# Kernel tuning notes

Hardware: AMD Instinct MI355X
Metric: run time of the kernel (lower is better)

## Reference

```python
import jax, jax.numpy as jnp
import numpy as np
from jax.ops import segment_sum

N_NODES = 10000
N_EDGES = 160000
HIDDEN = 128
NUM_RBF = 32
NUM_LAYERS = 2
LATENT = 64
N_GRAPHS = 128
CUTOFF = 5.0
EPS = 1e-8


def expnorm_rbf(r):
    # ExpNormalSmearing (ViSNet default RBF) with cosine cutoff
    means = jnp.linspace(jnp.exp(-CUTOFF), 1.0, NUM_RBF)          # [R]
    beta = (2.0 / NUM_RBF * (1.0 - jnp.exp(-CUTOFF))) ** -2
    cut = 0.5 * (jnp.cos(jnp.pi * r / CUTOFF) + 1.0) * (r < CUTOFF)
    return cut[:, None] * jnp.exp(-beta * (jnp.exp(-r)[:, None] - means) ** 2)  # [E,R]


def setup_inputs() -> dict:
    key = jax.random.key(0)
    ks = jax.random.split(key, 16)
    z = jax.random.randint(ks[0], (N_NODES,), 0, 100)
    pos = jax.random.normal(ks[1], (N_NODES, 3), jnp.float32) * 2.0
    batch = jnp.sort(jax.random.randint(ks[2], (N_NODES,), 0, N_GRAPHS))
    edge_index = jax.random.randint(ks[3], (2, N_EDGES), 0, N_NODES)
    H, R, L = HIDDEN, NUM_RBF, NUM_LAYERS
    s = lambda fan: 1.0 / np.sqrt(fan)
    embed_table = jax.random.normal(ks[4], (100, H), jnp.float32)
    W_rbf = jax.random.normal(ks[5], (L, R, H), jnp.float32) * s(R)
    W1 = jax.random.normal(ks[6], (L, H, H), jnp.float32) * s(H)
    Wo = jax.random.normal(ks[7], (L, H, H), jnp.float32) * s(H)
    Wv = jax.random.normal(ks[8], (L, H, H), jnp.float32) * s(H)
    Wvec1 = jax.random.normal(ks[9], (H, H), jnp.float32) * s(H)
    Wvec2 = jax.random.normal(ks[10], (H, H), jnp.float32) * s(H)
    W_a = jax.random.normal(ks[11], (2 * H, H), jnp.float32) * s(2 * H)
    b_a = jnp.zeros((H,), jnp.float32)
    W_b = jax.random.normal(ks[12], (H, LATENT + 1), jnp.float32) * s(H)
    b_b = jnp.zeros((LATENT + 1,), jnp.float32)
    # MSE-stability init fix from the torch module:
    # scalar_linear.bias[-1] = -1.0 ; scalar_linear.weight[-1] *= 0.1
    b_b = b_b.at[-1].set(-1.0)
    W_b = W_b.at[:, -1].multiply(0.1)
    return dict(z=z, pos=pos, batch=batch, edge_index=edge_index,
                embed_table=embed_table, W_rbf=W_rbf, W1=W1, Wo=Wo, Wv=Wv,
                Wvec1=Wvec1, Wvec2=Wvec2, W_a=W_a, b_a=b_a, W_b=W_b, b_b=b_b)


def reference(z, pos, batch, edge_index, embed_table, W_rbf, W1, Wo, Wv,
              Wvec1, Wvec2, W_a, b_a, W_b, b_b):
    src, dst = edge_index[0], edge_index[1]
    # edge geometry (computed once, shared across layers)
    d = pos[dst] - pos[src]                      # [E,3]
    r = jnp.sqrt(jnp.sum(d * d, axis=-1) + EPS)  # [E]
    dirn = d / r[:, None]                        # [E,3]
    rbf = expnorm_rbf(r)                         # [E,R]

    x = embed_table[z]                           # [N,H] scalar features
    vec = jnp.zeros((x.shape[0], 3, HIDDEN), x.dtype)  # [N,3,H] equivariant features

    for l in range(NUM_LAYERS):
        filt = rbf @ W_rbf[l]                                        # [E,H] radial filter
        phi = jax.nn.silu((x[src] * filt) @ W1[l])                   # [E,H] edge message
        dx = segment_sum(phi, dst, num_segments=N_NODES)             # scatter-add
        x = x + dx @ Wo[l]
        vmix = jnp.einsum('nch,hk->nck', vec, Wv[l])                 # [N,3,H]
        vmsg = vmix[src] * filt[:, None, :] + phi[:, None, :] * dirn[:, :, None]  # [E,3,H]
        vec = vec + segment_sum(vmsg, dst, num_segments=N_NODES)

    # gated-equivariant output head (pre_reduce -> [N, latent+1] scalars)
    v2 = jnp.einsum('nch,hk->nck', vec, Wvec2)
    vnorm = jnp.sqrt(jnp.sum(v2 * v2, axis=1) + EPS)                 # [N,H]
    a = jax.nn.silu(jnp.concatenate([x, vnorm], axis=-1) @ W_a + b_a)
    out = a @ W_b + b_b                                              # [N, latent+1]

    pooled = segment_sum(out, batch, num_segments=N_GRAPHS)          # global_add_pool
    mu = pooled[:, :LATENT]
    log_var = jnp.clip(pooled[:, LATENT:LATENT + 1], -10.0, 2.0)
    return mu, log_var
```

## Files before the change

kernel.cpp:

```cpp
#include <hip/hip_runtime.h>
#include <math.h>

#define N_NODES 10000
#define N_EDGES 160000
#define HIDDEN 128
#define NUM_RBF 32
#define LATENT 64
#define N_GRAPHS 128
#define CUTOFF 5.0f
#define EPS 1e-8f

#define NBLK_N 157

typedef __attribute__((ext_vector_type(8))) short short8;
typedef __attribute__((ext_vector_type(4))) float f32x4;
typedef unsigned short ushort_t;

__device__ __forceinline__ float fast_silu(float v) {
    return v * __builtin_amdgcn_rcpf(1.0f + __expf(-v));
}

__device__ __forceinline__ ushort_t f2bf(float f) {
    union { float f; unsigned u; } v;
    v.f = f;
    unsigned r = v.u + 0x7FFFu + ((v.u >> 16) & 1u);
    return (ushort_t)(r >> 16);
}
__device__ __forceinline__ float bf2f(ushort_t u) {
    union { unsigned u; float f; } v;
    v.u = ((unsigned)u) << 16;
    return v.f;
}

__global__ void init_kernel(const int* __restrict__ z, const float* __restrict__ embed,
                            float* __restrict__ x, ushort_t* __restrict__ x16,
                            float* __restrict__ vec, float* __restrict__ dxb,
                            float* __restrict__ pooled, int* __restrict__ deg,
                            const float* __restrict__ W1, const float* __restrict__ Wrbf,
                            const float* __restrict__ Wv, const float* __restrict__ Wo,
                            const float* __restrict__ Wvec2, const float* __restrict__ W_a,
                            const float* __restrict__ W_b, ushort_t* __restrict__ W1T,
                            ushort_t* __restrict__ WrbfT, ushort_t* __restrict__ WvT,
                            ushort_t* __restrict__ WoT, ushort_t* __restrict__ Wvec2T,
                            ushort_t* __restrict__ W_aT, ushort_t* __restrict__ W_bT) {
    if (blockIdx.x < 15000) {
        int i = blockIdx.x * 256 + threadIdx.x;
        if (i < N_NODES * 384) vec[i] = 0.0f;
        if (i < N_NODES * 128) {
            float v = embed[z[i >> 7] * 128 + (i & 127)];
            x[i] = v;
            x16[i] = f2bf(v);
            dxb[i] = 0.0f;
        }
        if (i < N_NODES) deg[i] = 0;
        if (i < N_GRAPHS * (LATENT + 1)) pooled[i] = 0.0f;
        return;
    }
    int i = (blockIdx.x - 15000) * 256 + threadIdx.x;
    if (i < 2 * 128 * 128) {
        int l = i >> 14;
        int n = (i & 16383) >> 7;
        int k = i & 127;
        W1T[i] = f2bf(W1[l * 16384 + k * 128 + n]);
        WvT[i] = f2bf(Wv[l * 16384 + k * 128 + n]);
        WoT[i] = f2bf(Wo[l * 16384 + k * 128 + n]);
    }
    if (i < 2 * 128 * 32) {
        int l = i >> 12;
        int n = (i & 4095) >> 5;
        int k = i & 31;
        WrbfT[i] = f2bf(Wrbf[l * 4096 + k * 128 + n]);
    }
    if (i < 128 * 128) {
        int n = i >> 7;
        int k = i & 127;
        Wvec2T[i] = f2bf(Wvec2[k * 128 + n]);
    }
    if (i < 128 * 256) {
        int n = i >> 8;
        int k = i & 255;
        W_aT[i] = f2bf(W_a[k * 128 + n]);
    }
    if (i < 80 * 128) {
        int n = i >> 7;
        int k = i & 127;
        W_bT[i] = (n < LATENT + 1) ? f2bf(W_b[k * (LATENT + 1) + n]) : (ushort_t)0;
    }
}

__global__ void hist_kernel(const int* __restrict__ dst, int* __restrict__ deg) {
    int e = blockIdx.x * blockDim.x + threadIdx.x;
    if (e < N_EDGES) atomicAdd(&deg[dst[e]], 1);
}

__global__ void prefix_kernel(const int* __restrict__ deg, int* __restrict__ cursor) {
    __shared__ int part[1024];
    const int ITEMS = 10;
    int t = threadIdx.x;
    int base = t * ITEMS;
    int local[ITEMS];
    int s = 0;
#pragma unroll
    for (int j = 0; j < ITEMS; j++) {
        int idx = base + j;
        int v = (idx < N_NODES) ? deg[idx] : 0;
        local[j] = s;
        s += v;
    }
    part[t] = s;
    __syncthreads();
    for (int off = 1; off < 1024; off <<= 1) {
        int v = (t >= off) ? part[t - off] : 0;
        __syncthreads();
        part[t] += v;
        __syncthreads();
    }
    int base_sum = (t > 0) ? part[t - 1] : 0;
#pragma unroll
    for (int j = 0; j < ITEMS; j++) {
        int idx = base + j;
        if (idx < N_NODES) cursor[idx] = base_sum + local[j];
    }
}

__global__ void scatter_geom_kernel(const int* __restrict__ ei, const float* __restrict__ pos,
                                    int* __restrict__ cursor, int* __restrict__ sperm,
                                    int* __restrict__ dperm, ushort_t* __restrict__ rbf16,
                                    float* __restrict__ dirn) {
    int e = blockIdx.x * blockDim.x + threadIdx.x;
    if (e >= N_EDGES) return;
    int s = ei[e];
    int t = ei[N_EDGES + e];
    int p = atomicAdd(&cursor[t], 1);
    sperm[p] = s;
    dperm[p] = t;

    float dx = pos[t * 3 + 0] - pos[s * 3 + 0];
    float dy = pos[t * 3 + 1] - pos[s * 3 + 1];
    float dz = pos[t * 3 + 2] - pos[s * 3 + 2];
    float r = sqrtf(dx * dx + dy * dy + dz * dz + EPS);
    float inv = 1.0f / r;
    dirn[p * 3 + 0] = dx * inv;
    dirn[p * 3 + 1] = dy * inv;
    dirn[p * 3 + 2] = dz * inv;

    float e5 = __expf(-CUTOFF);
    float span = 1.0f - e5;
    float b = (2.0f / NUM_RBF) * span;
    float beta = 1.0f / (b * b);
    float cut = (r < CUTOFF) ? 0.5f * (__cosf((float)M_PI * r / CUTOFF) + 1.0f) : 0.0f;
    float er = __expf(-r);
#pragma unroll
    for (int k = 0; k < NUM_RBF; k++) {
        float mean = e5 + span * ((float)k / (NUM_RBF - 1));
        float d = er - mean;
        rbf16[(size_t)p * 32 + k] = f2bf(cut * __expf(-beta * d * d));
    }
}

template <int K, int EPI>
__device__ __forceinline__ void gemm_body(ushort_t* As, float* __restrict__ A,
                                          const ushort_t* __restrict__ WT,
                                          const float* __restrict__ bias,
                                          const float* __restrict__ Cin, float* __restrict__ C,
                                          ushort_t* __restrict__ C16, int M, int bx, int tid) {
    constexpr int STR = K + 8;
    int row0 = bx * 64;
    int w = tid >> 6;
    int lane = tid & 63;
    int c = lane & 15;
    int q = lane >> 4;
    int wr0 = w * 16;

    {
        int r = wr0 + (lane >> 2);
        int row = row0 + r;
        int segbase = (lane & 3) * (K / 4);
#pragma unroll
        for (int u = 0; u < K / 16; u++) {
            int k0 = segbase + u * 4;
            float4 v = make_float4(0.f, 0.f, 0.f, 0.f);
            if (row < M) v = *(const float4*)(A + (size_t)row * 128 + k0);
            ushort_t b4[4] = {f2bf(v.x), f2bf(v.y), f2bf(v.z), f2bf(v.w)};
            *(uint2*)(As + r * STR + k0) = *(uint2*)b4;
        }
        if ((EPI & 16) && row < M) {
            float4 z4 = make_float4(0.f, 0.f, 0.f, 0.f);
#pragma unroll
            for (int u = 0; u < 8; u++)
                *(float4*)(A + (size_t)row * 128 + (lane & 3) * 32 + u * 4) = z4;
        }
    }

    f32x4 acc[8] = {};
#pragma unroll
    for (int s = 0; s < K / 32; s++) {
        short8 af = *(const short8*)(As + (wr0 + c) * STR + s * 32 + q * 8);
#pragma unroll
        for (int t8 = 0; t8 < 8; t8++) {
            short8 bf = *(const short8*)(WT + (size_t)(t8 * 16 + c) * K + s * 32 + q * 8);
            acc[t8] = __builtin_amdgcn_mfma_f32_16x16x32_bf16(af, bf, acc[t8], 0, 0, 0);
        }
    }

    if (EPI & 8) {
#pragma unroll
        for (int t8 = 0; t8 < 8; t8++) {
#pragma unroll
            for (int r4 = 0; r4 < 4; r4++) {
                int lrow = wr0 + q * 4 + r4;
                As[lrow * STR + t8 * 16 + c] = f2bf(acc[t8][r4]);
            }
        }
#pragma unroll
        for (int i = 0; i < 4; i++) {
            int slot = lane + i * 64;
            int rl = slot >> 4;
            int c8 = slot & 15;
            int row = row0 + wr0 + rl;
            if (row < M)
                *(uint4*)((ushort_t*)C + (size_t)row * 128 + c8 * 8) =
                    *(uint4*)(As + (wr0 + rl) * STR + c8 * 8);
        }
    } else {
#pragma unroll
        for (int t8 = 0; t8 < 8; t8++) {
#pragma unroll
            for (int r4 = 0; r4 < 4; r4++) {
                int row = row0 + wr0 + q * 4 + r4;
                if (row < M) {
                    int col = t8 * 16 + c;
                    float o = acc[t8][r4];
                    if (EPI & 1) o += bias[col];
                    if (EPI & 2) o += Cin[(size_t)row * 128 + col];
                    if (EPI & 4) o = fast_silu(o);
                    C[(size_t)row * 128 + col] = o;
                    if (EPI & 64) C16[(size_t)row * 128 + col] = f2bf(o);
                }
            }
        }
    }
}

__global__ __launch_bounds__(256, 4) void combo1_kernel(float* __restrict__ dxb,
                                                        const ushort_t* __restrict__ WoT0,
                                                        float* __restrict__ x,
                                                        ushort_t* __restrict__ x16,
                                                        float* __restrict__ vec,
                                                        const ushort_t* __restrict__ WvT1,
                                                        ushort_t* __restrict__ vmix16) {
    __shared__ ushort_t As[64 * 136];
    if (blockIdx.x < NBLK_N)
        gemm_body<128, 2 | 16 | 64>(As, dxb, WoT0, nullptr, x, x, x16, N_NODES, blockIdx.x,
                                    threadIdx.x);
    else
        gemm_body<128, 8>(As, vec, WvT1, nullptr, nullptr, (float*)vmix16, nullptr, N_NODES * 3,
                          blockIdx.x - NBLK_N, threadIdx.x);
}

__global__ __launch_bounds__(256, 4) void combo2_kernel(float* __restrict__ dxb,
                                                        const ushort_t* __restrict__ WoT1,
                                                        float* __restrict__ x,
                                                        float* __restrict__ vec,
                                                        const ushort_t* __restrict__ Wvec2T,
                                                        float* __restrict__ vbuf) {
    __shared__ ushort_t As[64 * 136];
    if (blockIdx.x < NBLK_N)
        gemm_body<128, 2>(As, dxb, WoT1, nullptr, x, x, nullptr, N_NODES, blockIdx.x,
                          threadIdx.x);
    else
        gemm_body<128, 0>(As, vec, Wvec2T, nullptr, nullptr, vbuf, nullptr, N_NODES * 3,
                          blockIdx.x - NBLK_N, threadIdx.x);
}

__global__ __launch_bounds__(256) void wa_pool_kernel(const float* __restrict__ x,
                                                      const float* __restrict__ vbuf,
                                                      const ushort_t* __restrict__ W_aT,
                                                      const float* __restrict__ b_a,
                                                      const ushort_t* __restrict__ W_bT,
                                                      const float* __restrict__ b_b,
                                                      const int* __restrict__ batch,
                                                      float* __restrict__ pooled) {
    __shared__ ushort_t As[16 * 264];
    __shared__ ushort_t A2[16 * 136];
    __shared__ int s_b[16];
    int tid = threadIdx.x;
    int row0 = blockIdx.x * 16;
    int w = tid >> 6;
    int lane = tid & 63;
    int c = lane & 15;
    int q = lane >> 4;

    if (tid < 16) s_b[tid] = batch[row0 + tid];
    {
        int r = tid >> 4;
        int seg = (tid & 15) * 16;
        int row = row0 + r;
#pragma unroll
        for (int u = 0; u < 4; u++) {
            int k0 = seg + u * 4;
            float4 v;
            if (k0 >= 128) {
                const float* vb = vbuf + (size_t)row * 384 + (k0 - 128);
                float4 va = *(const float4*)(vb);
                float4 vb2 = *(const float4*)(vb + 128);
                float4 vc = *(const float4*)(vb + 256);
                v.x = sqrtf(va.x * va.x + vb2.x * vb2.x + vc.x * vc.x + EPS);
                v.y = sqrtf(va.y * va.y + vb2.y * vb2.y + vc.y * vc.y + EPS);
                v.z = sqrtf(va.z * va.z + vb2.z * vb2.z + vc.z * vc.z + EPS);
                v.w = sqrtf(va.w * va.w + vb2.w * vb2.w + vc.w * vc.w + EPS);
            } else {
                v = *(const float4*)(x + (size_t)row * 128 + k0);
            }
            ushort_t b4[4] = {f2bf(v.x), f2bf(v.y), f2bf(v.z), f2bf(v.w)};
            *(uint2*)(As + r * 264 + k0) = *(uint2*)b4;
        }
    }
    __syncthreads();

    f32x4 acc[2] = {};
#pragma unroll
    for (int s = 0; s < 8; s++) {
        short8 af = *(const short8*)(As + c * 264 + s * 32 + q * 8);
#pragma unroll
        for (int i = 0; i < 2; i++) {
            int t8 = 2 * w + i;
            short8 bf = *(const short8*)(W_aT + (size_t)(t8 * 16 + c) * 256 + s * 32 + q * 8);
            acc[i] = __builtin_amdgcn_mfma_f32_16x16x32_bf16(af, bf, acc[i], 0, 0, 0);
        }
    }
#pragma unroll
    for (int i = 0; i < 2; i++) {
#pragma unroll
        for (int r4 = 0; r4 < 4; r4++) {
            int col = (2 * w + i) * 16 + c;
            A2[(q * 4 + r4) * 136 + col] = f2bf(fast_silu(acc[i][r4] + b_a[col]));
        }
    }
    __syncthreads();

    for (int t5 = w; t5 < 5; t5 += 4) {
        f32x4 acc2 = {};
#pragma unroll
        for (int s = 0; s < 4; s++) {
            short8 af = *(const short8*)(A2 + c * 136 + s * 32 + q * 8);
            short8 bf = *(const short8*)(W_bT + (size_t)(t5 * 16 + c) * 128 + s * 32 + q * 8);
            acc2 = __builtin_amdgcn_mfma_f32_16x16x32_bf16(af, bf, acc2, 0, 0, 0);
        }
        int col = t5 * 16 + c;
        if (col < LATENT + 1) {
            float bb = b_b[col];
#pragma unroll
            for (int r4 = 0; r4 < 4; r4++)
                atomicAdd(&pooled[s_b[q * 4 + r4] * (LATENT + 1) + col], acc2[r4] + bb);
        }
    }
}

template <bool HASV>
__global__ __launch_bounds__(256, 4) void edge_fused(
    const ushort_t* __restrict__ rbf16, const ushort_t* __restrict__ WrbfT,
    const ushort_t* __restrict__ x16, const int* __restrict__ sperm,
    const int* __restrict__ dperm, const ushort_t* __restrict__ W1T,
    const float* __restrict__ dirn, const ushort_t* __restrict__ vmix,
    float* __restrict__ dxb, float* __restrict__ vec) {
    __shared__ __align__(16) char smem_raw[HASV ? 36864 : 18432];
    ushort_t* Ts = (ushort_t*)smem_raw;
    ushort_t* PhiT = (ushort_t*)smem_raw;
    ushort_t* FiltT = (ushort_t*)(smem_raw + 18432);
    __shared__ __align__(16) int s_src[64];
    __shared__ __align__(16) int s_dst[64];
    __shared__ __align__(16) float s_dir4[256];

    int tid = threadIdx.x;
    int row0 = blockIdx.x * 64;
    int w = tid >> 6;
    int lane = tid & 63;
    int c = lane & 15;
    int q = lane >> 4;
    int wr0 = w * 16;

    if (lane < 16) {
        s_src[wr0 + lane] = sperm[row0 + wr0 + lane];
        s_dst[wr0 + lane] = dperm[row0 + wr0 + lane];
    }
    if (w == 3) {
        const float* dp = dirn + (size_t)(row0 + lane) * 3;
        s_dir4[lane * 4 + 0] = dp[0];
        s_dir4[lane * 4 + 1] = dp[1];
        s_dir4[lane * 4 + 2] = dp[2];
        s_dir4[lane * 4 + 3] = 0.f;
    }

    int srow[4];
#pragma unroll
    for (int r = 0; r < 4; r++) srow[r] = sperm[row0 + wr0 + q * 4 + r];
    ushort_t xv[4][8];
#pragma unroll
    for (int r = 0; r < 4; r++) {
        const ushort_t* xp = x16 + (size_t)srow[r] * 128 + c;
#pragma unroll
        for (int t8 = 0; t8 < 8; t8++) xv[r][t8] = xp[t8 * 16];
    }

    f32x4 facc[8];
    {
        short8 af = *(const short8*)(rbf16 + (size_t)(row0 + wr0 + c) * 32 + q * 8);
#pragma unroll
        for (int t8 = 0; t8 < 8; t8++) {
            short8 bfr = *(const short8*)(WrbfT + (size_t)(t8 * 16 + c) * 32 + q * 8);
            f32x4 z = {};
            facc[t8] = __builtin_amdgcn_mfma_f32_16x16x32_bf16(af, bfr, z, 0, 0, 0);
        }
    }

#pragma unroll
    for (int t8 = 0; t8 < 8; t8++) {
#pragma unroll
        for (int r = 0; r < 4; r++) {
            int row = wr0 + q * 4 + r;
            Ts[row * 136 + t8 * 16 + c] = f2bf(facc[t8][r] * bf2f(xv[r][t8]));
        }
    }

    f32x4 pacc[8] = {};
    const ushort_t* ap = Ts + (wr0 + c) * 136 + q * 8;
#pragma unroll
    for (int s = 0; s < 4; s++) {
        short8 af = *(const short8*)(ap + s * 32);
#pragma unroll
        for (int t8 = 0; t8 < 8; t8++) {
            short8 bfr = *(const short8*)(W1T + (size_t)(t8 * 16 + c) * 128 + s * 32 + q * 8);
            pacc[t8] = __builtin_amdgcn_mfma_f32_16x16x32_bf16(af, bfr, pacc[t8], 0, 0, 0);
        }
    }
    __syncthreads();

#pragma unroll
    for (int t8 = 0; t8 < 8; t8++) {
        int col = t8 * 16 + c;
        ushort_t pb[4];
#pragma unroll
        for (int r = 0; r < 4; r++) pb[r] = f2bf(fast_silu(pacc[t8][r]));
        *(uint2*)(PhiT + col * 72 + wr0 + q * 4) = *(uint2*)pb;
        if (HASV) {
            ushort_t fb[4];
#pragma unroll
            for (int r = 0; r < 4; r++) fb[r] = f2bf(facc[t8][r]);
            *(uint2*)(FiltT + col * 72 + wr0 + q * 4) = *(uint2*)fb;
        }
    }
    __syncthreads();

    int h = tid & 127;
    int half = tid >> 7;
    int rbeg = half * 32;
    float adx = 0.f, a0 = 0.f, a1 = 0.f, a2 = 0.f;

    float v0[2][8], v1[2][8], v2[2][8];
    if (HASV) {
        int sg[8];
        *(uint4*)&sg[0] = *(const uint4*)&s_src[rbeg];
        *(uint4*)&sg[4] = *(const uint4*)&s_src[rbeg + 4];
#pragma unroll
        for (int j = 0; j < 8; j++) {
            const ushort_t* vm = vmix + (size_t)sg[j] * 384 + h;
            v0[0][j] = bf2f(vm[0]);
            v1[0][j] = bf2f(vm[128]);
            v2[0][j] = bf2f(vm[256]);
        }
    }
    int cur = s_dst[rbeg];
#pragma unroll
    for (int g = 0; g < 4; g++) {
        int cb = g & 1, nb = cb ^ 1;
        if (HASV && g < 3) {
            int sg[8];
            *(uint4*)&sg[0] = *(const uint4*)&s_src[rbeg + (g + 1) * 8];
            *(uint4*)&sg[4] = *(const uint4*)&s_src[rbeg + (g + 1) * 8 + 4];
#pragma unroll
            for (int j = 0; j < 8; j++) {
                const ushort_t* vm = vmix + (size_t)sg[j] * 384 + h;
                v0[nb][j] = bf2f(vm[0]);
                v1[nb][j] = bf2f(vm[128]);
                v2[nb][j] = bf2f(vm[256]);
            }
        }
        int da[8];
        *(uint4*)&da[0] = *(const uint4*)&s_dst[rbeg + g * 8];
        *(uint4*)&da[4] = *(const uint4*)&s_dst[rbeg + g * 8 + 4];
        ushort_t ph[8], fl[8];
        *(uint4*)ph = *(const uint4*)(PhiT + h * 72 + rbeg + g * 8);
        if (HASV) *(uint4*)fl = *(const uint4*)(FiltT + h * 72 + rbeg + g * 8);
#pragma unroll
        for (int j = 0; j < 8; j++) {
            int r = rbeg + g * 8 + j;
            int d = da[j];
            if (d != cur) {
                atomicAdd(&dxb[(size_t)cur * 128 + h], adx);
                atomicAdd(&vec[((size_t)cur * 3 + 0) * 128 + h], a0);
                atomicAdd(&vec[((size_t)cur * 3 + 1) * 128 + h], a1);
                atomicAdd(&vec[((size_t)cur * 3 + 2) * 128 + h], a2);
                cur = d;
                adx = a0 = a1 = a2 = 0.f;
            }
            float p = bf2f(ph[j]);
            float4 dd = *(const float4*)(s_dir4 + r * 4);
            adx += p;
            if (HASV) {
                float f = bf2f(fl[j]);
                a0 += v0[cb][j] * f + p * dd.x;
                a1 += v1[cb][j] * f + p * dd.y;
                a2 += v2[cb][j] * f + p * dd.z;
            } else {
                a0 += p * dd.x;
                a1 += p * dd.y;
                a2 += p * dd.z;
            }
        }
    }
    atomicAdd(&dxb[(size_t)cur * 128 + h], adx);
    atomicAdd(&vec[((size_t)cur * 3 + 0) * 128 + h], a0);
    atomicAdd(&vec[((size_t)cur * 3 + 1) * 128 + h], a1);
    atomicAdd(&vec[((size_t)cur * 3 + 2) * 128 + h], a2);
}

__global__ void finalize_kernel(const float* __restrict__ pooled, float* __restrict__ out) {
    int i = blockIdx.x * blockDim.x + threadIdx.x;
    if (i >= N_GRAPHS * (LATENT + 1)) return;
    int g = i / (LATENT + 1);
    int k = i % (LATENT + 1);
    float v = pooled[i];
    if (k < LATENT) {
        out[g * LATENT + k] = v;
    } else {
        v = fminf(fmaxf(v, -10.0f), 2.0f);
        out[N_GRAPHS * LATENT + g] = v;
    }
}

extern "C" void kernel_launch(void* const* d_in, const int* in_sizes, int n_in,
                              void* d_out, int out_size, void* d_ws, size_t ws_size,
                              hipStream_t stream) {
    const int* z = (const int*)d_in[0];
    const float* pos = (const float*)d_in[1];
    const int* batch = (const int*)d_in[2];
    const int* ei = (const int*)d_in[3];
    const float* embed = (const float*)d_in[4];
    const float* W_rbf = (const float*)d_in[5];
    const float* W1 = (const float*)d_in[6];
    const float* Wo = (const float*)d_in[7];
    const float* Wv = (const float*)d_in[8];
    const float* Wvec2 = (const float*)d_in[10];
    const float* W_a = (const float*)d_in[11];
    const float* b_a = (const float*)d_in[12];
    const float* W_b = (const float*)d_in[13];
    const float* b_b = (const float*)d_in[14];
    float* out = (float*)d_out;

    const int* dsts = ei + N_EDGES;

    float* ws = (float*)d_ws;
    float* dirn = ws;
    float* x = dirn + (size_t)N_EDGES * 3;
    float* vec = x + (size_t)N_NODES * 128;
    float* vbuf = vec + (size_t)N_NODES * 384;
    float* dxb = vbuf + (size_t)N_NODES * 384;
    float* pooled = dxb + (size_t)N_NODES * 128;
    ushort_t* x16 = (ushort_t*)(pooled + N_GRAPHS * (LATENT + 1) + 16);
    ushort_t* rbf16 = x16 + (size_t)N_NODES * 128;
    ushort_t* vmix16 = rbf16 + (size_t)N_EDGES * 32;
    ushort_t* W1T = vmix16 + (size_t)N_NODES * 384;
    ushort_t* WrbfT = W1T + 2 * 16384;
    ushort_t* WvT = WrbfT + 2 * 4096;
    ushort_t* WoT = WvT + 2 * 16384;
    ushort_t* Wvec2T = WoT + 2 * 16384;
    ushort_t* W_aT = Wvec2T + 16384;
    ushort_t* W_bT = W_aT + 32768;
    int* ibase = (int*)(W_bT + 80 * 128);
    int* deg = ibase;
    int* cursor = deg + N_NODES;
    int* sperm = cursor + N_NODES;
    int* dperm = sperm + N_EDGES;

    init_kernel<<<15000 + 128, 256, 0, stream>>>(z, embed, x, x16, vec, dxb, pooled, deg, W1,
                                                 W_rbf, Wv, Wo, Wvec2, W_a, W_b, W1T, WrbfT, WvT,
                                                 WoT, Wvec2T, W_aT, W_bT);
    hist_kernel<<<(N_EDGES + 255) / 256, 256, 0, stream>>>(dsts, deg);
    prefix_kernel<<<1, 1024, 0, stream>>>(deg, cursor);
    scatter_geom_kernel<<<(N_EDGES + 255) / 256, 256, 0, stream>>>(ei, pos, cursor, sperm, dperm,
                                                                   rbf16, dirn);

    edge_fused<false><<<N_EDGES / 64, 256, 0, stream>>>(rbf16, WrbfT, x16, sperm, dperm, W1T,
                                                        dirn, nullptr, dxb, vec);
    combo1_kernel<<<NBLK_N + (N_NODES * 3 + 63) / 64, 256, 0, stream>>>(dxb, WoT, x, x16, vec,
                                                                        WvT + 16384, vmix16);
    edge_fused<true><<<N_EDGES / 64, 256, 0, stream>>>(rbf16, WrbfT + 4096, x16, sperm, dperm,
                                                       W1T + 16384, dirn, vmix16, dxb, vec);
    combo2_kernel<<<NBLK_N + (N_NODES * 3 + 63) / 64, 256, 0, stream>>>(dxb, WoT + 16384, x, vec,
                                                                        Wvec2T, vbuf);
    wa_pool_kernel<<<N_NODES / 16, 256, 0, stream>>>(x, vbuf, W_aT, b_a, W_bT, b_b, batch,
                                                     pooled);
    finalize_kernel<<<(N_GRAPHS * (LATENT + 1) + 255) / 256, 256, 0, stream>>>(pooled, out);
}
```

Baseline: 323.5 us.

## Compute edge geometry in original order, gather through permutation, memset zeroing

Edge geometry and RBF computation move into the histogram kernel and are stored in original edge order, so the scatter kernel only writes a small edge permutation plus src/dst indices. The edge kernels then load RBF rows and directions indirectly through the permutation. Zeroing of vec, dxb, pooled and deg moves from the init kernel to hipMemsetAsync calls, shrinking the init grid. The aim is to shorten the serial scatter step and make the RBF writes coalesced, at the cost of uncoalesced gathers in both edge passes and four extra memset launches.

After: 334.1 us. +3.3%, slower.

```diff
diff --git a/kernel.cpp b/kernel.cpp
--- a/kernel.cpp
+++ b/kernel.cpp
@@ -34,8 +34,6 @@
 
 __global__ void init_kernel(const int* __restrict__ z, const float* __restrict__ embed,
                             float* __restrict__ x, ushort_t* __restrict__ x16,
-                            float* __restrict__ vec, float* __restrict__ dxb,
-                            float* __restrict__ pooled, int* __restrict__ deg,
                             const float* __restrict__ W1, const float* __restrict__ Wrbf,
                             const float* __restrict__ Wv, const float* __restrict__ Wo,
                             const float* __restrict__ Wvec2, const float* __restrict__ W_a,
@@ -43,20 +41,16 @@
                             ushort_t* __restrict__ WrbfT, ushort_t* __restrict__ WvT,
                             ushort_t* __restrict__ WoT, ushort_t* __restrict__ Wvec2T,
                             ushort_t* __restrict__ W_aT, ushort_t* __restrict__ W_bT) {
-    if (blockIdx.x < 15000) {
+    if (blockIdx.x < 5000) {
         int i = blockIdx.x * 256 + threadIdx.x;
-        if (i < N_NODES * 384) vec[i] = 0.0f;
         if (i < N_NODES * 128) {
             float v = embed[z[i >> 7] * 128 + (i & 127)];
             x[i] = v;
             x16[i] = f2bf(v);
-            dxb[i] = 0.0f;
-        }
-        if (i < N_NODES) deg[i] = 0;
-        if (i < N_GRAPHS * (LATENT + 1)) pooled[i] = 0.0f;
+        }
         return;
     }
-    int i = (blockIdx.x - 15000) * 256 + threadIdx.x;
+    int i = (blockIdx.x - 5000) * 256 + threadIdx.x;
     if (i < 2 * 128 * 128) {
         int l = i >> 14;
         int n = (i & 16383) >> 7;
@@ -88,9 +82,36 @@
     }
 }
 
-__global__ void hist_kernel(const int* __restrict__ dst, int* __restrict__ deg) {
+__global__ void histgeom_kernel(const int* __restrict__ ei, const float* __restrict__ pos,
+                                int* __restrict__ deg, ushort_t* __restrict__ rbf16,
+                                float* __restrict__ dirn) {
     int e = blockIdx.x * blockDim.x + threadIdx.x;
-    if (e < N_EDGES) atomicAdd(&deg[dst[e]], 1);
+    if (e >= N_EDGES) return;
+    int s = ei[e];
+    int t = ei[N_EDGES + e];
+    atomicAdd(&deg[t], 1);
+
+    float dx = pos[t * 3 + 0] - pos[s * 3 + 0];
+    float dy = pos[t * 3 + 1] - pos[s * 3 + 1];
+    float dz = pos[t * 3 + 2] - pos[s * 3 + 2];
+    float r = sqrtf(dx * dx + dy * dy + dz * dz + EPS);
+    float inv = 1.0f / r;
+    dirn[e * 3 + 0] = dx * inv;
+    dirn[e * 3 + 1] = dy * inv;
+    dirn[e * 3 + 2] = dz * inv;
+
+    float e5 = __expf(-CUTOFF);
+    float span = 1.0f - e5;
+    float b = (2.0f / NUM_RBF) * span;
+    float beta = 1.0f / (b * b);
+    float cut = (r < CUTOFF) ? 0.5f * (__cosf((float)M_PI * r / CUTOFF) + 1.0f) : 0.0f;
+    float er = __expf(-r);
+#pragma unroll
+    for (int k = 0; k < NUM_RBF; k++) {
+        float mean = e5 + span * ((float)k / (NUM_RBF - 1));
+        float d = er - mean;
+        rbf16[(size_t)e * 32 + k] = f2bf(cut * __expf(-beta * d * d));
+    }
 }
 
 __global__ void prefix_kernel(const int* __restrict__ deg, int* __restrict__ cursor) {
@@ -123,38 +144,16 @@
     }
 }
 
-__global__ void scatter_geom_kernel(const int* __restrict__ ei, const float* __restrict__ pos,
-                                    int* __restrict__ cursor, int* __restrict__ sperm,
-                                    int* __restrict__ dperm, ushort_t* __restrict__ rbf16,
-                                    float* __restrict__ dirn) {
+__global__ void scatterperm_kernel(const int* __restrict__ ei, int* __restrict__ cursor,
+                                   int* __restrict__ eperm, int* __restrict__ sperm,
+                                   int* __restrict__ dperm) {
     int e = blockIdx.x * blockDim.x + threadIdx.x;
-    if (e >= N_EDGES) return;
-    int s = ei[e];
-    int t = ei[N_EDGES + e];
-    int p = atomicAdd(&cursor[t], 1);
-    sperm[p] = s;
-    dperm[p] = t;
-
-    float dx = pos[t * 3 + 0] - pos[s * 3 + 0];
-    float dy = pos[t * 3 + 1] - pos[s * 3 + 1];
-    float dz = pos[t * 3 + 2] - pos[s * 3 + 2];
-    float r = sqrtf(dx * dx + dy * dy + dz * dz + EPS);
-    float inv = 1.0f / r;
-    dirn[p * 3 + 0] = dx * inv;
-    dirn[p * 3 + 1] = dy * inv;
-    dirn[p * 3 + 2] = dz * inv;
-
-    float e5 = __expf(-CUTOFF);
-    float span = 1.0f - e5;
-    float b = (2.0f / NUM_RBF) * span;
-    float beta = 1.0f / (b * b);
-    float cut = (r < CUTOFF) ? 0.5f * (__cosf((float)M_PI * r / CUTOFF) + 1.0f) : 0.0f;
-    float er = __expf(-r);
-#pragma unroll
-    for (int k = 0; k < NUM_RBF; k++) {
-        float mean = e5 + span * ((float)k / (NUM_RBF - 1));
-        float d = er - mean;
-        rbf16[(size_t)p * 32 + k] = f2bf(cut * __expf(-beta * d * d));
+    if (e < N_EDGES) {
+        int d = ei[N_EDGES + e];
+        int p = atomicAdd(&cursor[d], 1);
+        eperm[p] = e;
+        sperm[p] = ei[e];
+        dperm[p] = d;
     }
 }
 
@@ -360,16 +359,17 @@
 template <bool HASV>
 __global__ __launch_bounds__(256, 4) void edge_fused(
     const ushort_t* __restrict__ rbf16, const ushort_t* __restrict__ WrbfT,
-    const ushort_t* __restrict__ x16, const int* __restrict__ sperm,
-    const int* __restrict__ dperm, const ushort_t* __restrict__ W1T,
-    const float* __restrict__ dirn, const ushort_t* __restrict__ vmix,
-    float* __restrict__ dxb, float* __restrict__ vec) {
+    const ushort_t* __restrict__ x16, const int* __restrict__ eperm,
+    const int* __restrict__ sperm, const int* __restrict__ dperm,
+    const ushort_t* __restrict__ W1T, const float* __restrict__ dirn,
+    const ushort_t* __restrict__ vmix, float* __restrict__ dxb, float* __restrict__ vec) {
     __shared__ __align__(16) char smem_raw[HASV ? 36864 : 18432];
     ushort_t* Ts = (ushort_t*)smem_raw;
     ushort_t* PhiT = (ushort_t*)smem_raw;
     ushort_t* FiltT = (ushort_t*)(smem_raw + 18432);
     __shared__ __align__(16) int s_src[64];
     __shared__ __align__(16) int s_dst[64];
+    __shared__ __align__(16) int s_ep[64];
     __shared__ __align__(16) float s_dir4[256];
 
     int tid = threadIdx.x;
@@ -383,9 +383,11 @@
     if (lane < 16) {
         s_src[wr0 + lane] = sperm[row0 + wr0 + lane];
         s_dst[wr0 + lane] = dperm[row0 + wr0 + lane];
+        s_ep[wr0 + lane] = eperm[row0 + wr0 + lane];
     }
     if (w == 3) {
-        const float* dp = dirn + (size_t)(row0 + lane) * 3;
+        int ep3 = eperm[row0 + lane];
+        const float* dp = dirn + (size_t)ep3 * 3;
         s_dir4[lane * 4 + 0] = dp[0];
         s_dir4[lane * 4 + 1] = dp[1];
         s_dir4[lane * 4 + 2] = dp[2];
@@ -405,7 +407,7 @@
 
     f32x4 facc[8];
     {
-        short8 af = *(const short8*)(rbf16 + (size_t)(row0 + wr0 + c) * 32 + q * 8);
+        short8 af = *(const short8*)(rbf16 + (size_t)s_ep[wr0 + c] * 32 + q * 8);
 #pragma unroll
         for (int t8 = 0; t8 < 8; t8++) {
             short8 bfr = *(const short8*)(WrbfT + (size_t)(t8 * 16 + c) * 32 + q * 8);
@@ -558,8 +560,6 @@
     const float* b_b = (const float*)d_in[14];
     float* out = (float*)d_out;
 
-    const int* dsts = ei + N_EDGES;
-
     float* ws = (float*)d_ws;
     float* dirn = ws;
     float* x = dirn + (size_t)N_EDGES * 3;
@@ -580,23 +580,29 @@
     int* ibase = (int*)(W_bT + 80 * 128);
     int* deg = ibase;
     int* cursor = deg + N_NODES;
-    int* sperm = cursor + N_NODES;
+    int* eperm = cursor + N_NODES;
+    int* sperm = eperm + N_EDGES;
     int* dperm = sperm + N_EDGES;
 
-    init_kernel<<<15000 + 128, 256, 0, stream>>>(z, embed, x, x16, vec, dxb, pooled, deg, W1,
-                                                 W_rbf, Wv, Wo, Wvec2, W_a, W_b, W1T, WrbfT, WvT,
-                                                 WoT, Wvec2T, W_aT, W_bT);
-    hist_kernel<<<(N_EDGES + 255) / 256, 256, 0, stream>>>(dsts, deg);
+    hipMemsetAsync(vec, 0, (size_t)N_NODES * 384 * 4, stream);
+    hipMemsetAsync(dxb, 0, (size_t)N_NODES * 128 * 4, stream);
+    hipMemsetAsync(pooled, 0, (size_t)N_GRAPHS * (LATENT + 1) * 4, stream);
+    hipMemsetAsync(deg, 0, (size_t)N_NODES * 4, stream);
+
+    init_kernel<<<5000 + 128, 256, 0, stream>>>(z, embed, x, x16, W1, W_rbf, Wv, Wo, Wvec2, W_a,
+                                                W_b, W1T, WrbfT, WvT, WoT, Wvec2T, W_aT, W_bT);
+    histgeom_kernel<<<(N_EDGES + 255) / 256, 256, 0, stream>>>(ei, pos, deg, rbf16, dirn);
     prefix_kernel<<<1, 1024, 0, stream>>>(deg, cursor);
-    scatter_geom_kernel<<<(N_EDGES + 255) / 256, 256, 0, stream>>>(ei, pos, cursor, sperm, dperm,
-                                                                   rbf16, dirn);
-
-    edge_fused<false><<<N_EDGES / 64, 256, 0, stream>>>(rbf16, WrbfT, x16, sperm, dperm, W1T,
-                                                        dirn, nullptr, dxb, vec);
+    scatterperm_kernel<<<(N_EDGES + 255) / 256, 256, 0, stream>>>(ei, cursor, eperm, sperm,
+                                                                  dperm);
+
+    edge_fused<false><<<N_EDGES / 64, 256, 0, stream>>>(rbf16, WrbfT, x16, eperm, sperm, dperm,
+                                                        W1T, dirn, nullptr, dxb, vec);
     combo1_kernel<<<NBLK_N + (N_NODES * 3 + 63) / 64, 256, 0, stream>>>(dxb, WoT, x, x16, vec,
                                                                         WvT + 16384, vmix16);
-    edge_fused<true><<<N_EDGES / 64, 256, 0, stream>>>(rbf16, WrbfT + 4096, x16, sperm, dperm,
-                                                       W1T + 16384, dirn, vmix16, dxb, vec);
+    edge_fused<true><<<N_EDGES / 64, 256, 0, stream>>>(rbf16, WrbfT + 4096, x16, eperm, sperm,
+                                                       dperm, W1T + 16384, dirn, vmix16, dxb,
+                                                       vec);
     combo2_kernel<<<NBLK_N + (N_NODES * 3 + 63) / 64, 256, 0, stream>>>(dxb, WoT + 16384, x, vec,
                                                                         Wvec2T, vbuf);
     wa_pool_kernel<<<N_NODES / 16, 256, 0, stream>>>(x, vbuf, W_aT, b_a, W_bT, b_b, batch,
```

## Prefetch vmix gathers at kernel start and drop shared src/dst index staging

Applied to the files above, without the earlier changes.

The edge kernel now issues the gather of the first two groups of vmix rows (bf16, kept in registers) at the very start, before the GEMM phase, so their latency overlaps the matmul work. Later groups are prefetched two groups ahead in a ring buffer. The s_src/s_dst shared arrays are removed and indices are read directly from global memory. This holds 48 raw bf16 values live across the GEMM, which raises register pressure and could lower occupancy under the 256x4 launch bound.

After: 377.5 us. 16.7% more time.

```diff
diff --git a/kernel.cpp b/kernel.cpp
--- a/kernel.cpp
+++ b/kernel.cpp
@@ -368,8 +368,6 @@
     ushort_t* Ts = (ushort_t*)smem_raw;
     ushort_t* PhiT = (ushort_t*)smem_raw;
     ushort_t* FiltT = (ushort_t*)(smem_raw + 18432);
-    __shared__ __align__(16) int s_src[64];
-    __shared__ __align__(16) int s_dst[64];
     __shared__ __align__(16) float s_dir4[256];
 
     int tid = threadIdx.x;
@@ -379,11 +377,25 @@
     int c = lane & 15;
     int q = lane >> 4;
     int wr0 = w * 16;
-
-    if (lane < 16) {
-        s_src[wr0 + lane] = sperm[row0 + wr0 + lane];
-        s_dst[wr0 + lane] = dperm[row0 + wr0 + lane];
-    }
+    int h = tid & 127;
+    int half = tid >> 7;
+    int rbeg = half * 32;
+
+    ushort_t pr0[2][8], pr1[2][8], pr2[2][8];
+    if (HASV) {
+#pragma unroll
+        for (int g = 0; g < 2; g++) {
+#pragma unroll
+            for (int j = 0; j < 8; j++) {
+                int sidx = sperm[row0 + rbeg + g * 8 + j];
+                const ushort_t* vm = vmix + (size_t)sidx * 384 + h;
+                pr0[g][j] = vm[0];
+                pr1[g][j] = vm[128];
+                pr2[g][j] = vm[256];
+            }
+        }
+    }
+
     if (w == 3) {
         const float* dp = dirn + (size_t)(row0 + lane) * 3;
         s_dir4[lane * 4 + 0] = dp[0];
@@ -452,43 +464,33 @@
     }
     __syncthreads();
 
-    int h = tid & 127;
-    int half = tid >> 7;
-    int rbeg = half * 32;
     float adx = 0.f, a0 = 0.f, a1 = 0.f, a2 = 0.f;
-
-    float v0[2][8], v1[2][8], v2[2][8];
-    if (HASV) {
-        int sg[8];
-        *(uint4*)&sg[0] = *(const uint4*)&s_src[rbeg];
-        *(uint4*)&sg[4] = *(const uint4*)&s_src[rbeg + 4];
-#pragma unroll
-        for (int j = 0; j < 8; j++) {
-            const ushort_t* vm = vmix + (size_t)sg[j] * 384 + h;
-            v0[0][j] = bf2f(vm[0]);
-            v1[0][j] = bf2f(vm[128]);
-            v2[0][j] = bf2f(vm[256]);
-        }
-    }
-    int cur = s_dst[rbeg];
+    int cur = dperm[row0 + rbeg];
 #pragma unroll
     for (int g = 0; g < 4; g++) {
-        int cb = g & 1, nb = cb ^ 1;
-        if (HASV && g < 3) {
-            int sg[8];
-            *(uint4*)&sg[0] = *(const uint4*)&s_src[rbeg + (g + 1) * 8];
-            *(uint4*)&sg[4] = *(const uint4*)&s_src[rbeg + (g + 1) * 8 + 4];
+        int b = g & 1;
+        float v0[8], v1[8], v2[8];
+        if (HASV) {
 #pragma unroll
             for (int j = 0; j < 8; j++) {
-                const ushort_t* vm = vmix + (size_t)sg[j] * 384 + h;
-                v0[nb][j] = bf2f(vm[0]);
-                v1[nb][j] = bf2f(vm[128]);
-                v2[nb][j] = bf2f(vm[256]);
+                v0[j] = bf2f(pr0[b][j]);
+                v1[j] = bf2f(pr1[b][j]);
+                v2[j] = bf2f(pr2[b][j]);
+            }
+            if (g < 2) {
+#pragma unroll
+                for (int j = 0; j < 8; j++) {
+                    int sidx = sperm[row0 + rbeg + (g + 2) * 8 + j];
+                    const ushort_t* vm = vmix + (size_t)sidx * 384 + h;
+                    pr0[b][j] = vm[0];
+                    pr1[b][j] = vm[128];
+                    pr2[b][j] = vm[256];
+                }
             }
         }
         int da[8];
-        *(uint4*)&da[0] = *(const uint4*)&s_dst[rbeg + g * 8];
-        *(uint4*)&da[4] = *(const uint4*)&s_dst[rbeg + g * 8 + 4];
+        *(uint4*)&da[0] = *(const uint4*)(dperm + row0 + rbeg + g * 8);
+        *(uint4*)&da[4] = *(const uint4*)(dperm + row0 + rbeg + g * 8 + 4);
         ushort_t ph[8], fl[8];
         *(uint4*)ph = *(const uint4*)(PhiT + h * 72 + rbeg + g * 8);
         if (HASV) *(uint4*)fl = *(const uint4*)(FiltT + h * 72 + rbeg + g * 8);
@@ -509,9 +511,9 @@
             adx += p;
             if (HASV) {
                 float f = bf2f(fl[j]);
-                a0 += v0[cb][j] * f + p * dd.x;
-                a1 += v1[cb][j] * f + p * dd.y;
-                a2 += v2[cb][j] * f + p * dd.z;
+                a0 += v0[j] * f + p * dd.x;
+                a1 += v1[j] * f + p * dd.y;
+                a2 += v2[j] * f + p * dd.z;
             } else {
                 a0 += p * dd.x;
                 a1 += p * dd.y;
```
